# Kernel optimization log

Measured on AMD Instinct MI355X. Metric: run time of the kernel, lower is better.

## Reference

```python
import jax, jax.numpy as jnp
import numpy as np

NCLASS = 19
BETA = 0.999
IGNORE = -1


def setup_inputs() -> dict:
    key = jax.random.key(0)
    k1, k2 = jax.random.split(key)
    logits = jax.random.normal(k1, (8, NCLASS, 512, 1024), dtype=jnp.float32)
    target = jax.random.randint(k2, (8, 512, 1024), 0, NCLASS, dtype=jnp.int32)
    return {"logits": logits, "target": target}


def _class_balanced_weights(target):
    # Vectorized replacement of the per-sample torch.histc loop.
    B = target.shape[0]
    t = target.reshape(B, -1)
    valid = (t >= 0) & (t < NCLASS)  # histc drops out-of-range (e.g. -1)
    seg = jnp.where(valid, jnp.arange(B, dtype=t.dtype)[:, None] * NCLASS + t, B * NCLASS)
    counts = jax.ops.segment_sum(
        jnp.ones(seg.size, dtype=jnp.float32), seg.reshape(-1),
        num_segments=B * NCLASS + 1)[: B * NCLASS].reshape(B, NCLASS)
    total = counts.sum(axis=0)  # [NCLASS] class counts over whole batch
    w = (1.0 - BETA) / (1.0 - jnp.power(jnp.float32(BETA), total))
    # torch code zeroes the inf entries (classes with zero count)
    return jnp.where(total > 0, w, 0.0)


def reference(logits, target):
    weights = _class_balanced_weights(target)  # [NCLASS]
    logp = jax.nn.log_softmax(logits, axis=1)  # [B, C, H, W]
    tc = jnp.clip(target, 0, NCLASS - 1)
    tgt_logp = jnp.take_along_axis(logp, tc[:, None].astype(jnp.int32), axis=1)[:, 0]  # [B, H, W]
    valid = (target != IGNORE).astype(logits.dtype)
    w_t = weights[tc] * valid  # per-pixel class weight, 0 at ignored pixels
    # PyTorch weighted cross_entropy 'mean': sum(w*nll) / sum(w) over valid
    loss = -(w_t * tgt_logp).sum() / w_t.sum()
    return loss
```

## Files before the change

kernel.cpp:

```cpp
#include <hip/hip_runtime.h>
#include <math.h>

#define NCLASS 19
#define IGNORE_LBL (-1)

constexpr int BDIM   = 8;
constexpr int HWDIM  = 512 * 1024;
constexpr int NPIX   = BDIM * HWDIM;
constexpr int NSTRIP = BDIM * NCLASS;
constexpr int PIXB   = 1024;
constexpr int RING   = 8;
constexpr int DEPTH  = 6;
constexpr double BETA = 0.999;

struct WS {
    double num;
    double den;
    int    counts[NCLASS];
    float  weights[NCLASS];
};

__global__ void init_ws(WS* ws) {
    int t = threadIdx.x;
    if (t == 0) { ws->num = 0.0; ws->den = 0.0; }
    if (t < NCLASS) ws->counts[t] = 0;
}

__global__ void hist_kernel(const int* __restrict__ tgt, WS* __restrict__ ws, int n4) {
    __shared__ int sh[NCLASS];
    if (threadIdx.x < NCLASS) sh[threadIdx.x] = 0;
    __syncthreads();
    int stride = gridDim.x * blockDim.x;
    for (int i = blockIdx.x * blockDim.x + threadIdx.x; i < n4; i += stride) {
        int4 t = reinterpret_cast<const int4*>(tgt)[i];
        if (t.x >= 0 && t.x < NCLASS) atomicAdd(&sh[t.x], 1);
        if (t.y >= 0 && t.y < NCLASS) atomicAdd(&sh[t.y], 1);
        if (t.z >= 0 && t.z < NCLASS) atomicAdd(&sh[t.z], 1);
        if (t.w >= 0 && t.w < NCLASS) atomicAdd(&sh[t.w], 1);
    }
    __syncthreads();
    if (threadIdx.x < NCLASS && sh[threadIdx.x] != 0)
        atomicAdd(&ws->counts[threadIdx.x], sh[threadIdx.x]);
}

__global__ void weights_kernel(WS* ws) {
    int c = threadIdx.x;
    if (c < NCLASS) {
        double total = (double)ws->counts[c];
        float w = 0.0f;
        if (total > 0.0) {
            double p = exp(total * log(BETA));
            w = (float)((1.0 - BETA) / (1.0 - p));
        }
        ws->weights[c] = w;
    }
}

typedef const __attribute__((address_space(1))) void* as1_t;
typedef __attribute__((address_space(3))) void*       as3_t;

__device__ __forceinline__ void gload16(const float* g, float* l) {
    __builtin_amdgcn_global_load_lds((as1_t)g, (as3_t)l, 16, 0, 0);
}

__global__ __launch_bounds__(256)
void loss_kernel(const float* __restrict__ logits, const int* __restrict__ tgt,
                 WS* __restrict__ ws) {
    __shared__ __align__(16) float ring[RING][PIXB];
    __shared__ float  s_w[NCLASS];
    __shared__ double sh_n[4], sh_d[4];

    const int  tid = threadIdx.x;
    const int  wid = tid >> 6;
    const long px0 = (long)blockIdx.x * PIXB;

    if (tid < NCLASS) s_w[tid] = ws->weights[tid];
    __syncthreads();

    int4 t_cur = *reinterpret_cast<const int4*>(tgt + px0 + 4 * tid);

    const float* gissue = logits + px0 + wid * 256;
    const float* glast  = logits + px0 + (long)(NSTRIP - 1) * HWDIM + wid * 256;

#pragma unroll
    for (int s = 0; s < DEPTH; ++s) {
        gload16(gissue, &ring[s][wid * 256]);
        gissue += HWDIM;
    }

    float num = 0.f, den = 0.f;
    int slot = 0;

#pragma unroll 1
    for (int b = 0; b < BDIM; ++b) {
        int4 t_nxt = t_cur;
        if (b + 1 < BDIM)
            t_nxt = *reinterpret_cast<const int4*>(
                tgt + (long)(b + 1) * HWDIM + px0 + 4 * tid);

        float s0 = 0.f, s1 = 0.f, s2 = 0.f, s3 = 0.f;
        float ta0 = 0.f, ta1 = 0.f, ta2 = 0.f, ta3 = 0.f;

#pragma unroll
        for (int c = 0; c < NCLASS; ++c) {
            gload16(gissue, &ring[(slot + DEPTH) & (RING - 1)][wid * 256]);
            if (gissue < glast) gissue += HWDIM;
            asm volatile("s_waitcnt vmcnt(6)" ::: "memory");
            __builtin_amdgcn_sched_barrier(0);

            float4 v = *reinterpret_cast<const float4*>(&ring[slot][4 * tid]);
            s0 += __expf(v.x);
            s1 += __expf(v.y);
            s2 += __expf(v.z);
            s3 += __expf(v.w);
            if (c == t_cur.x) ta0 = v.x;
            if (c == t_cur.y) ta1 = v.y;
            if (c == t_cur.z) ta2 = v.z;
            if (c == t_cur.w) ta3 = v.w;
            slot = (slot + 1) & (RING - 1);
        }

        int tc; float w;
        tc = min(max(t_cur.x, 0), NCLASS - 1); w = (t_cur.x != IGNORE_LBL) ? s_w[tc] : 0.f;
        num += w * (ta0 - __logf(s0)); den += w;
        tc = min(max(t_cur.y, 0), NCLASS - 1); w = (t_cur.y != IGNORE_LBL) ? s_w[tc] : 0.f;
        num += w * (ta1 - __logf(s1)); den += w;
        tc = min(max(t_cur.z, 0), NCLASS - 1); w = (t_cur.z != IGNORE_LBL) ? s_w[tc] : 0.f;
        num += w * (ta2 - __logf(s2)); den += w;
        tc = min(max(t_cur.w, 0), NCLASS - 1); w = (t_cur.w != IGNORE_LBL) ? s_w[tc] : 0.f;
        num += w * (ta3 - __logf(s3)); den += w;

        t_cur = t_nxt;
    }

#pragma unroll
    for (int off = 32; off > 0; off >>= 1) {
        num += __shfl_down(num, off);
        den += __shfl_down(den, off);
    }
    int lane = tid & 63;
    if (lane == 0) { sh_n[wid] = (double)num; sh_d[wid] = (double)den; }
    __syncthreads();
    if (tid == 0) {
        double n = sh_n[0] + sh_n[1] + sh_n[2] + sh_n[3];
        double d = sh_d[0] + sh_d[1] + sh_d[2] + sh_d[3];
        atomicAdd(&ws->num, n);
        atomicAdd(&ws->den, d);
    }
}

__global__ void finalize_kernel(const WS* __restrict__ ws, float* __restrict__ out) {
    if (threadIdx.x == 0) {
        out[0] = (float)(-(ws->num / ws->den));
    }
}

extern "C" void kernel_launch(void* const* d_in, const int* in_sizes, int n_in,
                              void* d_out, int out_size, void* d_ws, size_t ws_size,
                              hipStream_t stream) {
    const float* logits = (const float*)d_in[0];
    const int*   target = (const int*)d_in[1];
    float*       out    = (float*)d_out;
    WS*          ws     = (WS*)d_ws;

    init_ws<<<1, 64, 0, stream>>>(ws);
    hist_kernel<<<1024, 256, 0, stream>>>(target, ws, NPIX / 4);
    weights_kernel<<<1, 32, 0, stream>>>(ws);
    loss_kernel<<<HWDIM / PIXB, 256, 0, stream>>>(logits, target, ws);
    finalize_kernel<<<1, 1, 0, stream>>>(ws, out);
}
```

Measured before the change: 83.32 us.

## Fuse histogram into loss pass via per-class NLL sums, apply weights at finalize

Because each pixel's weight depends only on its class, the loss is rewritten as a sum over classes of w_c times the per-class NLL sum, divided by a sum of w_c times the class count. The loss kernel accumulates per-class NLL sums and counts in shared memory with LDS atomics, and the finalize kernel computes the weights and combines them. This removes the separate histogram pass over the targets and the weights kernel, saving two launches and a full read of the target tensor. In exchange it adds contended shared-memory atomics with only 19 bins in the inner loop and float accumulation of per-block partial sums.

Measured after the change: 80.29 us. 1.04x faster.

```diff
diff --git a/kernel.cpp b/kernel.cpp
--- a/kernel.cpp
+++ b/kernel.cpp
@@ -14,46 +14,13 @@
 constexpr double BETA = 0.999;
 
 struct WS {
-    double num;
-    double den;
+    double sums[NCLASS];
     int    counts[NCLASS];
-    float  weights[NCLASS];
 };
 
 __global__ void init_ws(WS* ws) {
     int t = threadIdx.x;
-    if (t == 0) { ws->num = 0.0; ws->den = 0.0; }
-    if (t < NCLASS) ws->counts[t] = 0;
-}
-
-__global__ void hist_kernel(const int* __restrict__ tgt, WS* __restrict__ ws, int n4) {
-    __shared__ int sh[NCLASS];
-    if (threadIdx.x < NCLASS) sh[threadIdx.x] = 0;
-    __syncthreads();
-    int stride = gridDim.x * blockDim.x;
-    for (int i = blockIdx.x * blockDim.x + threadIdx.x; i < n4; i += stride) {
-        int4 t = reinterpret_cast<const int4*>(tgt)[i];
-        if (t.x >= 0 && t.x < NCLASS) atomicAdd(&sh[t.x], 1);
-        if (t.y >= 0 && t.y < NCLASS) atomicAdd(&sh[t.y], 1);
-        if (t.z >= 0 && t.z < NCLASS) atomicAdd(&sh[t.z], 1);
-        if (t.w >= 0 && t.w < NCLASS) atomicAdd(&sh[t.w], 1);
-    }
-    __syncthreads();
-    if (threadIdx.x < NCLASS && sh[threadIdx.x] != 0)
-        atomicAdd(&ws->counts[threadIdx.x], sh[threadIdx.x]);
-}
-
-__global__ void weights_kernel(WS* ws) {
-    int c = threadIdx.x;
-    if (c < NCLASS) {
-        double total = (double)ws->counts[c];
-        float w = 0.0f;
-        if (total > 0.0) {
-            double p = exp(total * log(BETA));
-            w = (float)((1.0 - BETA) / (1.0 - p));
-        }
-        ws->weights[c] = w;
-    }
+    if (t < NCLASS) { ws->sums[t] = 0.0; ws->counts[t] = 0; }
 }
 
 typedef const __attribute__((address_space(1))) void* as1_t;
@@ -64,17 +31,17 @@
 }
 
 __global__ __launch_bounds__(256)
-void loss_kernel(const float* __restrict__ logits, const int* __restrict__ tgt,
-                 WS* __restrict__ ws) {
+void loss_fused_kernel(const float* __restrict__ logits, const int* __restrict__ tgt,
+                       WS* __restrict__ ws) {
     __shared__ __align__(16) float ring[RING][PIXB];
-    __shared__ float  s_w[NCLASS];
-    __shared__ double sh_n[4], sh_d[4];
+    __shared__ float l_sum[NCLASS];
+    __shared__ int   l_cnt[NCLASS];
 
     const int  tid = threadIdx.x;
     const int  wid = tid >> 6;
     const long px0 = (long)blockIdx.x * PIXB;
 
-    if (tid < NCLASS) s_w[tid] = ws->weights[tid];
+    if (tid < NCLASS) { l_sum[tid] = 0.f; l_cnt[tid] = 0; }
     __syncthreads();
 
     int4 t_cur = *reinterpret_cast<const int4*>(tgt + px0 + 4 * tid);
@@ -88,7 +55,6 @@
         gissue += HWDIM;
     }
 
-    float num = 0.f, den = 0.f;
     int slot = 0;
 
 #pragma unroll 1
@@ -120,38 +86,45 @@
             slot = (slot + 1) & (RING - 1);
         }
 
-        int tc; float w;
-        tc = min(max(t_cur.x, 0), NCLASS - 1); w = (t_cur.x != IGNORE_LBL) ? s_w[tc] : 0.f;
-        num += w * (ta0 - __logf(s0)); den += w;
-        tc = min(max(t_cur.y, 0), NCLASS - 1); w = (t_cur.y != IGNORE_LBL) ? s_w[tc] : 0.f;
-        num += w * (ta1 - __logf(s1)); den += w;
-        tc = min(max(t_cur.z, 0), NCLASS - 1); w = (t_cur.z != IGNORE_LBL) ? s_w[tc] : 0.f;
-        num += w * (ta2 - __logf(s2)); den += w;
-        tc = min(max(t_cur.w, 0), NCLASS - 1); w = (t_cur.w != IGNORE_LBL) ? s_w[tc] : 0.f;
-        num += w * (ta3 - __logf(s3)); den += w;
+        if (t_cur.x >= 0 && t_cur.x < NCLASS) {
+            atomicAdd(&l_sum[t_cur.x], ta0 - __logf(s0));
+            atomicAdd(&l_cnt[t_cur.x], 1);
+        }
+        if (t_cur.y >= 0 && t_cur.y < NCLASS) {
+            atomicAdd(&l_sum[t_cur.y], ta1 - __logf(s1));
+            atomicAdd(&l_cnt[t_cur.y], 1);
+        }
+        if (t_cur.z >= 0 && t_cur.z < NCLASS) {
+            atomicAdd(&l_sum[t_cur.z], ta2 - __logf(s2));
+            atomicAdd(&l_cnt[t_cur.z], 1);
+        }
+        if (t_cur.w >= 0 && t_cur.w < NCLASS) {
+            atomicAdd(&l_sum[t_cur.w], ta3 - __logf(s3));
+            atomicAdd(&l_cnt[t_cur.w], 1);
+        }
 
         t_cur = t_nxt;
     }
 
-#pragma unroll
-    for (int off = 32; off > 0; off >>= 1) {
-        num += __shfl_down(num, off);
-        den += __shfl_down(den, off);
-    }
-    int lane = tid & 63;
-    if (lane == 0) { sh_n[wid] = (double)num; sh_d[wid] = (double)den; }
     __syncthreads();
-    if (tid == 0) {
-        double n = sh_n[0] + sh_n[1] + sh_n[2] + sh_n[3];
-        double d = sh_d[0] + sh_d[1] + sh_d[2] + sh_d[3];
-        atomicAdd(&ws->num, n);
-        atomicAdd(&ws->den, d);
+    if (tid < NCLASS) {
+        atomicAdd(&ws->sums[tid], (double)l_sum[tid]);
+        atomicAdd(&ws->counts[tid], l_cnt[tid]);
     }
 }
 
 __global__ void finalize_kernel(const WS* __restrict__ ws, float* __restrict__ out) {
     if (threadIdx.x == 0) {
-        out[0] = (float)(-(ws->num / ws->den));
+        double num = 0.0, den = 0.0;
+        for (int c = 0; c < NCLASS; ++c) {
+            double n = (double)ws->counts[c];
+            if (n > 0.0) {
+                double w = (1.0 - BETA) / (1.0 - exp(n * log(BETA)));
+                num += w * ws->sums[c];
+                den += w * n;
+            }
+        }
+        out[0] = (float)(-(num / den));
     }
 }
 
@@ -163,9 +136,7 @@
     float*       out    = (float*)d_out;
     WS*          ws     = (WS*)d_ws;
 
-    init_ws<<<1, 64, 0, stream>>>(ws);
-    hist_kernel<<<1024, 256, 0, stream>>>(target, ws, NPIX / 4);
-    weights_kernel<<<1, 32, 0, stream>>>(ws);
-    loss_kernel<<<HWDIM / PIXB, 256, 0, stream>>>(logits, target, ws);
+    init_ws<<<1, 32, 0, stream>>>(ws);
+    loss_fused_kernel<<<HWDIM / PIXB, 256, 0, stream>>>(logits, target, ws);
     finalize_kernel<<<1, 1, 0, stream>>>(ws, out);
 }
```
